# Kernel optimization log

Hardware: AMD Instinct MI355X
Metric: run time of the kernel (lower is better)

The kernel has to match this reference:

```python
import jax, jax.numpy as jnp
import numpy as np
from jax import lax

BETA = 0.95
THRESHOLD = 1.0
B, T, D_IN, D_OUT = 128, 512, 512, 512


def setup_inputs() -> dict:
    key = jax.random.key(0)
    k1, k2, k3 = jax.random.split(key, 3)
    x_seq = jax.random.normal(k1, (B, T, D_IN), dtype=jnp.float32)
    W = jax.random.normal(k2, (D_OUT, D_IN), dtype=jnp.float32) * (1.0 / np.sqrt(D_IN))
    b = jax.random.normal(k3, (D_OUT,), dtype=jnp.float32) * 0.01
    return {"x_seq": x_seq, "W": W, "b": b}


def reference(x_seq, W, b):
    # Batch the linear across all timesteps: [B,T,D_in] @ [D_out,D_in]^T -> [B,T,D_out]
    currents = jnp.einsum('bti,oi->bto', x_seq, W) + b

    def step(mem, cur):  # mem: [B, D_out], cur: [B, D_out]
        mem = BETA * mem + cur
        spk = (mem > THRESHOLD).astype(mem.dtype)
        return mem - spk * THRESHOLD, spk

    mem0 = jnp.zeros((x_seq.shape[0], W.shape[0]), dtype=x_seq.dtype)
    _, spikes_tbd = lax.scan(step, mem0, jnp.swapaxes(currents, 0, 1))  # [T,B,D]
    spikes = jnp.swapaxes(spikes_tbd, 0, 1)  # [B,T,D]
    return spikes, spikes.sum()
```

## Files before the change

kernel.cpp:

```cpp
#include <hip/hip_runtime.h>
#include <hip/hip_bf16.h>

#define M_TOT 65536
#define K_DIM 512
#define N_DIM 512
#define T_STEPS 512
#define BETA 0.95f

#define BM 128
#define BN 128
#define BK 64

typedef __attribute__((ext_vector_type(8))) short bf16x8;
typedef __attribute__((ext_vector_type(4))) float f32x4;

static __device__ __forceinline__ unsigned short f2bf(float f) {
    __hip_bfloat16 h = __float2bfloat16(f);
    return __builtin_bit_cast(unsigned short, h);
}

static __device__ __forceinline__ void stage_tiles(
    unsigned short (*__restrict__ Xs)[BK], unsigned short (*__restrict__ Ws)[BK],
    const float4* xr, const float4* wv, int sr0, int skg)
{
    #pragma unroll
    for (int i = 0; i < 8; ++i) {
        int r   = sr0 + i * 16;
        int kgs = skg ^ ((r & 7) << 3);
        ushort4 xb, wb;
        xb.x = f2bf(xr[i].x); xb.y = f2bf(xr[i].y); xb.z = f2bf(xr[i].z); xb.w = f2bf(xr[i].w);
        wb.x = f2bf(wv[i].x); wb.y = f2bf(wv[i].y); wb.z = f2bf(wv[i].z); wb.w = f2bf(wv[i].w);
        *(ushort4*)(&Xs[r][kgs]) = xb;
        *(ushort4*)(&Ws[r][kgs]) = wb;
    }
}

__global__ __launch_bounds__(256, 2) void gemm_currents(
    const float* __restrict__ X,
    const float* __restrict__ W,
    const float* __restrict__ bias,
    float* __restrict__ C,
    float* __restrict__ sum_out)
{
    __shared__ unsigned short Xs[2][BM][BK];
    __shared__ unsigned short Ws[2][BN][BK];

    const int lin  = blockIdx.x;
    const int swz  = (lin & 7) * 256 + (lin >> 3);
    const int mtile = swz >> 2;
    const int ntile = swz & 3;

    const int tid  = threadIdx.x;
    const int lane = tid & 63;
    const int wave = tid >> 6;
    const int wr = wave >> 1;
    const int wc = wave & 1;

    if (lin == 0 && tid == 0) *sum_out = 0.0f;

    const int row0 = mtile * BM;
    const int col0 = ntile * BN;

    f32x4 acc[4][4] = {};

    const int sr0 = tid >> 4;
    const int skg = (tid & 15) << 2;
    const float* xbase = X + (size_t)row0 * K_DIM + skg;
    const float* wbase = W + (size_t)col0 * K_DIM + skg;

    float4 xr[8], wv[8];

    #pragma unroll
    for (int i = 0; i < 8; ++i) {
        int r = sr0 + i * 16;
        xr[i] = *(const float4*)(xbase + (size_t)r * K_DIM);
        wv[i] = *(const float4*)(wbase + (size_t)r * K_DIM);
    }
    stage_tiles(Xs[0], Ws[0], xr, wv, sr0, skg);

    const int frow = lane & 15;
    const int cblk = lane >> 4;

    for (int t = 0; t < 8; ++t) {
        __syncthreads();

        if (t < 7) {
            const int k0n = (t + 1) * BK;
            #pragma unroll
            for (int i = 0; i < 8; ++i) {
                int r = sr0 + i * 16;
                xr[i] = *(const float4*)(xbase + (size_t)r * K_DIM + k0n);
                wv[i] = *(const float4*)(wbase + (size_t)r * K_DIM + k0n);
            }
        }

        unsigned short (*Xb)[BK] = Xs[t & 1];
        unsigned short (*Wb)[BK] = Ws[t & 1];
        #pragma unroll
        for (int kh = 0; kh < 2; ++kh) {
            bf16x8 afr[4], bfr[4];
            #pragma unroll
            for (int m = 0; m < 4; ++m) {
                int row = wr * 64 + m * 16 + frow;
                int c = (kh * 4 + cblk) ^ (row & 7);
                afr[m] = *(const bf16x8*)(&Xb[row][c * 8]);
            }
            #pragma unroll
            for (int n = 0; n < 4; ++n) {
                int row = wc * 64 + n * 16 + frow;
                int c = (kh * 4 + cblk) ^ (row & 7);
                bfr[n] = *(const bf16x8*)(&Wb[row][c * 8]);
            }
            #pragma unroll
            for (int m = 0; m < 4; ++m)
                #pragma unroll
                for (int n = 0; n < 4; ++n)
                    acc[m][n] = __builtin_amdgcn_mfma_f32_16x16x32_bf16(
                        afr[m], bfr[n], acc[m][n], 0, 0, 0);
        }

        if (t < 7)
            stage_tiles(Xs[(t + 1) & 1], Ws[(t + 1) & 1], xr, wv, sr0, skg);
    }

    const int crow_base = (lane >> 4) * 4;
    const int ccol = lane & 15;
    #pragma unroll
    for (int n = 0; n < 4; ++n) {
        int col = col0 + wc * 64 + n * 16 + ccol;
        float bv = bias[col];
        #pragma unroll
        for (int m = 0; m < 4; ++m) {
            int rowb = row0 + wr * 64 + m * 16 + crow_base;
            #pragma unroll
            for (int r = 0; r < 4; ++r) {
                C[(size_t)(rowb + r) * N_DIM + col] = acc[m][n][r] + bv;
            }
        }
    }
}

__global__ __launch_bounds__(256) void lif_scan(
    float* __restrict__ C,
    float* __restrict__ sum_out)
{
    const int idx = blockIdx.x * 256 + threadIdx.x;
    float* p = C + (size_t)(idx >> 9) * (T_STEPS * N_DIM) + (idx & 511);

    float mem = 0.0f;
    int count = 0;
    float a[16], b[16];

    #pragma unroll
    for (int j = 0; j < 16; ++j)
        a[j] = p[(size_t)j * N_DIM];

    for (int t = 0; t < T_STEPS; t += 32) {
        #pragma unroll
        for (int j = 0; j < 16; ++j)
            b[j] = p[(size_t)(t + 16 + j) * N_DIM];
        #pragma unroll
        for (int j = 0; j < 16; ++j) {
            mem = BETA * mem + a[j];
            float spk = (mem > 1.0f) ? 1.0f : 0.0f;
            mem -= spk;
            __builtin_nontemporal_store(spk, p + (size_t)(t + j) * N_DIM);
            count += (int)spk;
        }
        if (t + 32 < T_STEPS) {
            #pragma unroll
            for (int j = 0; j < 16; ++j)
                a[j] = p[(size_t)(t + 32 + j) * N_DIM];
        }
        #pragma unroll
        for (int j = 0; j < 16; ++j) {
            mem = BETA * mem + b[j];
            float spk = (mem > 1.0f) ? 1.0f : 0.0f;
            mem -= spk;
            __builtin_nontemporal_store(spk, p + (size_t)(t + 16 + j) * N_DIM);
            count += (int)spk;
        }
    }

    #pragma unroll
    for (int off = 32; off > 0; off >>= 1)
        count += __shfl_down(count, off);
    __shared__ int wsum[4];
    if ((threadIdx.x & 63) == 0) wsum[threadIdx.x >> 6] = count;
    __syncthreads();
    if (threadIdx.x == 0) {
        int tot = wsum[0] + wsum[1] + wsum[2] + wsum[3];
        atomicAdd(sum_out, (float)tot);
    }
}

extern "C" void kernel_launch(void* const* d_in, const int* in_sizes, int n_in,
                              void* d_out, int out_size, void* d_ws, size_t ws_size,
                              hipStream_t stream) {
    const float* X    = (const float*)d_in[0];
    const float* W    = (const float*)d_in[1];
    const float* bias = (const float*)d_in[2];
    float* out = (float*)d_out;
    float* sum_slot = out + (size_t)M_TOT * N_DIM;

    gemm_currents<<<(M_TOT / BM) * (N_DIM / BN), 256, 0, stream>>>(X, W, bias, out, sum_slot);
    lif_scan<<<M_TOT / 256, 256, 0, stream>>>(out, sum_slot);
}
```

Before: 333.5 us.

## Pre-convert inputs to bf16 in workspace and use direct global-to-LDS GEMM loads

Adds a conversion kernel that writes bf16 copies of X and W into the workspace, then a GEMM that streams those tiles straight into LDS with global_load_lds, removing per-thread fp32-to-bf16 conversion and register staging from the GEMM loop. The old fused-conversion GEMM is kept as a fallback when the workspace is too small. The LIF scan prefetch depth is doubled to 32 timesteps. This trades an extra full pass writing and reading a bf16 copy of X, plus a single-buffered LDS pipeline, for a lighter GEMM inner loop.

```diff
diff --git a/kernel.cpp b/kernel.cpp
--- a/kernel.cpp
+++ b/kernel.cpp
@@ -12,11 +12,139 @@
 #define BK 64
 
 typedef __attribute__((ext_vector_type(8))) short bf16x8;
+typedef __attribute__((ext_vector_type(8))) unsigned short u16x8;
 typedef __attribute__((ext_vector_type(4))) float f32x4;
+
+#define X_ELEMS ((size_t)M_TOT * K_DIM)
+#define W_ELEMS ((size_t)N_DIM * K_DIM)
+#define WS_NEEDED ((X_ELEMS + W_ELEMS) * 2)
 
 static __device__ __forceinline__ unsigned short f2bf(float f) {
     __hip_bfloat16 h = __float2bfloat16(f);
     return __builtin_bit_cast(unsigned short, h);
+}
+
+__global__ __launch_bounds__(256) void convert_bf16(
+    const float* __restrict__ X, const float* __restrict__ W,
+    unsigned short* __restrict__ Xb, unsigned short* __restrict__ Wb,
+    float* __restrict__ sum_out)
+{
+    const size_t gid = (size_t)blockIdx.x * 256 + threadIdx.x;
+    if (gid == 0) *sum_out = 0.0f;
+    const size_t NXT = X_ELEMS / 8;
+    if (gid < NXT) {
+        const float4 v0 = *(const float4*)(X + gid * 8);
+        const float4 v1 = *(const float4*)(X + gid * 8 + 4);
+        u16x8 o;
+        o[0] = f2bf(v0.x); o[1] = f2bf(v0.y); o[2] = f2bf(v0.z); o[3] = f2bf(v0.w);
+        o[4] = f2bf(v1.x); o[5] = f2bf(v1.y); o[6] = f2bf(v1.z); o[7] = f2bf(v1.w);
+        *(u16x8*)(Xb + gid * 8) = o;
+    } else {
+        const size_t g2 = gid - NXT;
+        const float4 v0 = *(const float4*)(W + g2 * 8);
+        const float4 v1 = *(const float4*)(W + g2 * 8 + 4);
+        u16x8 o;
+        o[0] = f2bf(v0.x); o[1] = f2bf(v0.y); o[2] = f2bf(v0.z); o[3] = f2bf(v0.w);
+        o[4] = f2bf(v1.x); o[5] = f2bf(v1.y); o[6] = f2bf(v1.z); o[7] = f2bf(v1.w);
+        *(u16x8*)(Wb + g2 * 8) = o;
+    }
+}
+
+__global__ __launch_bounds__(256) void gemm_fast(
+    const unsigned short* __restrict__ Xb,
+    const unsigned short* __restrict__ Wb,
+    const float* __restrict__ bias,
+    float* __restrict__ C)
+{
+    __shared__ alignas(16) unsigned short Xs[BM][BK];
+    __shared__ alignas(16) unsigned short Ws[BN][BK];
+
+    const int lin  = blockIdx.x;
+    const int swz  = (lin & 7) * 256 + (lin >> 3);
+    const int mtile = swz >> 2;
+    const int ntile = swz & 3;
+
+    const int tid  = threadIdx.x;
+    const int lane = tid & 63;
+    const int wave = tid >> 6;
+    const int wr = wave >> 1;
+    const int wc = wave & 1;
+
+    const int row0 = mtile * BM;
+    const int col0 = ntile * BN;
+
+    f32x4 acc[4][4] = {};
+
+    const int srow = lane >> 3;
+    const int scb  = (lane & 7) ^ (srow & 7);
+    const unsigned short* xsrc[4];
+    const unsigned short* wsrc[4];
+    #pragma unroll
+    for (int j = 0; j < 4; ++j) {
+        const int ra = row0 + wave * 32 + j * 8 + srow;
+        const int rb = col0 + wave * 32 + j * 8 + srow;
+        xsrc[j] = Xb + (size_t)ra * K_DIM + scb * 8;
+        wsrc[j] = Wb + (size_t)rb * K_DIM + scb * 8;
+    }
+
+    const int frow = lane & 15;
+    const int cblk = lane >> 4;
+
+    #pragma unroll
+    for (int t = 0; t < 8; ++t) {
+        if (t) __syncthreads();
+        #pragma unroll
+        for (int j = 0; j < 4; ++j) {
+            __builtin_amdgcn_global_load_lds(
+                (const __attribute__((address_space(1))) unsigned int*)(const void*)(xsrc[j] + t * BK),
+                (__attribute__((address_space(3))) unsigned int*)(void*)(&Xs[wave * 32 + j * 8][0]),
+                16, 0, 0);
+            __builtin_amdgcn_global_load_lds(
+                (const __attribute__((address_space(1))) unsigned int*)(const void*)(wsrc[j] + t * BK),
+                (__attribute__((address_space(3))) unsigned int*)(void*)(&Ws[wave * 32 + j * 8][0]),
+                16, 0, 0);
+        }
+        __syncthreads();
+
+        #pragma unroll
+        for (int kh = 0; kh < 2; ++kh) {
+            bf16x8 afr[4], bfr[4];
+            #pragma unroll
+            for (int m = 0; m < 4; ++m) {
+                int row = wr * 64 + m * 16 + frow;
+                int c = (kh * 4 + cblk) ^ (row & 7);
+                afr[m] = *(const bf16x8*)(&Xs[row][c * 8]);
+            }
+            #pragma unroll
+            for (int n = 0; n < 4; ++n) {
+                int row = wc * 64 + n * 16 + frow;
+                int c = (kh * 4 + cblk) ^ (row & 7);
+                bfr[n] = *(const bf16x8*)(&Ws[row][c * 8]);
+            }
+            #pragma unroll
+            for (int m = 0; m < 4; ++m)
+                #pragma unroll
+                for (int n = 0; n < 4; ++n)
+                    acc[m][n] = __builtin_amdgcn_mfma_f32_16x16x32_bf16(
+                        afr[m], bfr[n], acc[m][n], 0, 0, 0);
+        }
+    }
+
+    const int crow_base = (lane >> 4) * 4;
+    const int ccol = lane & 15;
+    #pragma unroll
+    for (int n = 0; n < 4; ++n) {
+        int col = col0 + wc * 64 + n * 16 + ccol;
+        float bv = bias[col];
+        #pragma unroll
+        for (int m = 0; m < 4; ++m) {
+            int rowb = row0 + wr * 64 + m * 16 + crow_base;
+            #pragma unroll
+            for (int r = 0; r < 4; ++r) {
+                C[(size_t)(rowb + r) * N_DIM + col] = acc[m][n][r] + bv;
+            }
+        }
+    }
 }
 
 static __device__ __forceinline__ void stage_tiles(
@@ -35,11 +163,9 @@
     }
 }
 
-__global__ __launch_bounds__(256, 2) void gemm_currents(
-    const float* __restrict__ X,
-    const float* __restrict__ W,
-    const float* __restrict__ bias,
-    float* __restrict__ C,
+__global__ __launch_bounds__(256, 2) void gemm_slow(
+    const float* __restrict__ X, const float* __restrict__ W,
+    const float* __restrict__ bias, float* __restrict__ C,
     float* __restrict__ sum_out)
 {
     __shared__ unsigned short Xs[2][BM][BK];
@@ -69,7 +195,6 @@
     const float* wbase = W + (size_t)col0 * K_DIM + skg;
 
     float4 xr[8], wv[8];
-
     #pragma unroll
     for (int i = 0; i < 8; ++i) {
         int r = sr0 + i * 16;
@@ -83,7 +208,6 @@
 
     for (int t = 0; t < 8; ++t) {
         __syncthreads();
-
         if (t < 7) {
             const int k0n = (t + 1) * BK;
             #pragma unroll
@@ -93,7 +217,6 @@
                 wv[i] = *(const float4*)(wbase + (size_t)r * K_DIM + k0n);
             }
         }
-
         unsigned short (*Xb)[BK] = Xs[t & 1];
         unsigned short (*Wb)[BK] = Ws[t & 1];
         #pragma unroll
@@ -118,7 +241,6 @@
                     acc[m][n] = __builtin_amdgcn_mfma_f32_16x16x32_bf16(
                         afr[m], bfr[n], acc[m][n], 0, 0, 0);
         }
-
         if (t < 7)
             stage_tiles(Xs[(t + 1) & 1], Ws[(t + 1) & 1], xr, wv, sr0, skg);
     }
@@ -149,35 +271,35 @@
 
     float mem = 0.0f;
     int count = 0;
-    float a[16], b[16];
-
-    #pragma unroll
-    for (int j = 0; j < 16; ++j)
+    float a[32], b[32];
+
+    #pragma unroll
+    for (int j = 0; j < 32; ++j)
         a[j] = p[(size_t)j * N_DIM];
 
-    for (int t = 0; t < T_STEPS; t += 32) {
-        #pragma unroll
-        for (int j = 0; j < 16; ++j)
-            b[j] = p[(size_t)(t + 16 + j) * N_DIM];
-        #pragma unroll
-        for (int j = 0; j < 16; ++j) {
+    for (int t = 0; t < T_STEPS; t += 64) {
+        #pragma unroll
+        for (int j = 0; j < 32; ++j)
+            b[j] = p[(size_t)(t + 32 + j) * N_DIM];
+        #pragma unroll
+        for (int j = 0; j < 32; ++j) {
             mem = BETA * mem + a[j];
             float spk = (mem > 1.0f) ? 1.0f : 0.0f;
             mem -= spk;
             __builtin_nontemporal_store(spk, p + (size_t)(t + j) * N_DIM);
             count += (int)spk;
         }
-        if (t + 32 < T_STEPS) {
-            #pragma unroll
-            for (int j = 0; j < 16; ++j)
-                a[j] = p[(size_t)(t + 32 + j) * N_DIM];
-        }
-        #pragma unroll
-        for (int j = 0; j < 16; ++j) {
+        if (t + 64 < T_STEPS) {
+            #pragma unroll
+            for (int j = 0; j < 32; ++j)
+                a[j] = p[(size_t)(t + 64 + j) * N_DIM];
+        }
+        #pragma unroll
+        for (int j = 0; j < 32; ++j) {
             mem = BETA * mem + b[j];
             float spk = (mem > 1.0f) ? 1.0f : 0.0f;
             mem -= spk;
-            __builtin_nontemporal_store(spk, p + (size_t)(t + 16 + j) * N_DIM);
+            __builtin_nontemporal_store(spk, p + (size_t)(t + 32 + j) * N_DIM);
             count += (int)spk;
         }
     }
@@ -203,6 +325,14 @@
     float* out = (float*)d_out;
     float* sum_slot = out + (size_t)M_TOT * N_DIM;
 
-    gemm_currents<<<(M_TOT / BM) * (N_DIM / BN), 256, 0, stream>>>(X, W, bias, out, sum_slot);
+    if (ws_size >= WS_NEEDED) {
+        unsigned short* Xb = (unsigned short*)d_ws;
+        unsigned short* Wb = Xb + X_ELEMS;
+        const int nconv = (int)((X_ELEMS / 8 + W_ELEMS / 8) / 256);
+        convert_bf16<<<nconv, 256, 0, stream>>>(X, W, Xb, Wb, sum_slot);
+        gemm_fast<<<(M_TOT / BM) * (N_DIM / BN), 256, 0, stream>>>(Xb, Wb, bias, out);
+    } else {
+        gemm_slow<<<(M_TOT / BM) * (N_DIM / BN), 256, 0, stream>>>(X, W, bias, out, sum_slot);
+    }
     lif_scan<<<M_TOT / 256, 256, 0, stream>>>(out, sum_slot);
 }
```

Measured after the change: 315.5 us. 5.4% less time.
